# Performance work log

Measured on AMD Instinct MI355X. Metric: run time of the kernel, lower is better.

Reference implementation:

```python
import jax, jax.numpy as jnp
import numpy as np

D_MODEL = 1024
N_HEADS = 16
D_K = D_MODEL // N_HEADS  # 64
B, T = 2, 2048


def setup_inputs() -> dict:
    key = jax.random.key(0)
    ks = jax.random.split(key, 6)
    s = 0.02
    x = jax.random.normal(ks[0], (B, T, D_MODEL), dtype=jnp.float32)
    # Stacked per-head projection weights, [H, C, d_k] (no bias, mini-gpt style)
    Wq = jax.random.normal(ks[1], (N_HEADS, D_MODEL, D_K), dtype=jnp.float32) * s
    Wk = jax.random.normal(ks[2], (N_HEADS, D_MODEL, D_K), dtype=jnp.float32) * s
    Wv = jax.random.normal(ks[3], (N_HEADS, D_MODEL, D_K), dtype=jnp.float32) * s
    # Output projection, torch nn.Linear(d_model, d_model): y = x @ Wo.T + bo
    Wo = jax.random.normal(ks[4], (D_MODEL, D_MODEL), dtype=jnp.float32) * s
    bo = jax.random.normal(ks[5], (D_MODEL,), dtype=jnp.float32) * s
    return {"x": x, "Wq": Wq, "Wk": Wk, "Wv": Wv, "Wo": Wo, "bo": bo}


def reference(x, Wq, Wk, Wv, Wo, bo):
    Bq, Tq, C = x.shape
    # Batched per-head projections (replaces the per-head Python loop)
    q = jnp.einsum('btc,hck->bhtk', x, Wq)  # [B,H,T,dk]
    k = jnp.einsum('btc,hck->bhtk', x, Wk)
    v = jnp.einsum('btc,hck->bhtk', x, Wv)
    scale = 1.0 / jnp.sqrt(jnp.asarray(D_K, dtype=x.dtype))
    scores = jnp.einsum('bhtk,bhsk->bhts', q, k) * scale  # [B,H,T,T]
    causal = jnp.tril(jnp.ones((Tq, Tq), dtype=bool))
    scores = jnp.where(causal, scores, jnp.asarray(-1e9, dtype=scores.dtype))
    attn = jax.nn.softmax(scores, axis=-1)
    out = jnp.einsum('bhts,bhsk->bhtk', attn, v)  # [B,H,T,dk]
    # concat heads -> [B,T,C]
    out = out.transpose(0, 2, 1, 3).reshape(Bq, Tq, C)
    return jnp.einsum('btc,dc->btd', out, Wo) + bo
```

## Files before the change

kernel.cpp:

```cpp
#include <hip/hip_runtime.h>
#include <hip/hip_bf16.h>


using short8 = __attribute__((ext_vector_type(8))) short;
using f32x4  = __attribute__((ext_vector_type(4))) float;
using fp16x2 = __attribute__((ext_vector_type(2))) __fp16;
using half4  = __attribute__((ext_vector_type(4))) _Float16;
using half8  = __attribute__((ext_vector_type(8))) _Float16;

#define SCALE_LOG2E 0.18033688011112042f

__device__ __forceinline__ unsigned short f2bf(float f) {
    union { float f; unsigned u; } v; v.f = f;
    unsigned r = v.u + 0x7fffu + ((v.u >> 16) & 1u);
    return (unsigned short)(r >> 16);
}

__device__ __forceinline__ void gld16(const unsigned short* gp, unsigned short* lp) {
    __builtin_amdgcn_global_load_lds(
        (const __attribute__((address_space(1))) void*)(gp),
        (__attribute__((address_space(3))) void*)(unsigned int)(unsigned long long)(lp),
        16, 0, 0);
}

__global__ void cvt_bf16(const float* __restrict__ in,
                         unsigned short* __restrict__ out, int n4) {
    int i = blockIdx.x * blockDim.x + threadIdx.x;
    if (i >= n4) return;
    float4 v = ((const float4*)in)[i];
    ushort4 o;
    o.x = f2bf(v.x); o.y = f2bf(v.y); o.z = f2bf(v.z); o.w = f2bf(v.w);
    ((ushort4*)out)[i] = o;
}

__global__ void transpose_w(const float* __restrict__ Wq,
                            const float* __restrict__ Wk,
                            const float* __restrict__ Wv,
                            unsigned short* __restrict__ out) {
    __shared__ float tile[64][65];
    int b = blockIdx.x;
    int cchunk = b & 15;
    int h = (b >> 4) & 15;
    int s = b >> 8;
    const float* W = (s == 0) ? Wq : ((s == 1) ? Wk : Wv);
    float sc = (s == 0) ? SCALE_LOG2E : 1.0f;
    const float* src = W + (h * 1024 + cchunk * 64) * 64;
    int t = threadIdx.x;
    #pragma unroll
    for (int it = 0; it < 4; ++it) {
        int idx = (it * 256 + t) * 4;
        int cc = idx >> 6, kk = idx & 63;
        float4 v = *(const float4*)(src + idx);
        tile[cc][kk + 0] = v.x; tile[cc][kk + 1] = v.y;
        tile[cc][kk + 2] = v.z; tile[cc][kk + 3] = v.w;
    }
    __syncthreads();
    unsigned short* dst = out + (size_t)((s * 16 + h) * 64) * 1024 + cchunk * 64;
    #pragma unroll
    for (int it = 0; it < 16; ++it) {
        int idx = it * 256 + t;
        int kk = idx >> 6, cc = idx & 63;
        dst[kk * 1024 + cc] = f2bf(tile[cc][kk] * sc);
    }
}

__global__ __launch_bounds__(256, 5) void qkv_gemm(
        const unsigned short* __restrict__ xb,
        const unsigned short* __restrict__ Wt,
        unsigned short* __restrict__ qB,
        unsigned short* __restrict__ kfrag,
        _Float16* __restrict__ vfrag) {
    __shared__ unsigned short Als[128 * 32];
    __shared__ unsigned short Bls[64 * 32];
    int wave = threadIdx.x >> 6;
    int lane = threadIdx.x & 63;
    int col  = lane & 15;
    int quad = lane >> 4;
    int m_off = (wave & 1) * 64;
    int n_off = (wave >> 1) * 32;
    int ldr = lane >> 2;
    int ldc = ((lane & 3) ^ ((lane >> 3) & 3)) * 8;
    int swq = (quad ^ ((col >> 1) & 3)) * 8;
    int m0 = blockIdx.x * 128;
    int n0 = blockIdx.y * 64;
    f32x4 acc[4][2] = {};
    for (int k0 = 0; k0 < 1024; k0 += 32) {
        __syncthreads();
        #pragma unroll
        for (int j = 0; j < 2; ++j) {
            int row = wave * 32 + j * 16;
            gld16(xb + (size_t)(m0 + row + ldr) * 1024 + k0 + ldc, Als + row * 32);
        }
        {
            int row = wave * 16;
            gld16(Wt + (size_t)(n0 + row + ldr) * 1024 + k0 + ldc, Bls + row * 32);
        }
        __syncthreads();
        short8 af[4], bf[2];
        #pragma unroll
        for (int i = 0; i < 4; ++i)
            af[i] = *(const short8*)(Als + (m_off + i * 16 + col) * 32 + swq);
        #pragma unroll
        for (int i = 0; i < 2; ++i)
            bf[i] = *(const short8*)(Bls + (n_off + i * 16 + col) * 32 + swq);
        #pragma unroll
        for (int mb = 0; mb < 4; ++mb)
            #pragma unroll
            for (int nb = 0; nb < 2; ++nb)
                acc[mb][nb] = __builtin_amdgcn_mfma_f32_16x16x32_bf16(
                    af[mb], bf[nb], acc[mb][nb], 0, 0, 0);
    }
    int sel = blockIdx.y >> 4;
    #pragma unroll
    for (int nb = 0; nb < 2; ++nb) {
        int n = n0 + n_off + nb * 16 + col;
        int d10 = n & 1023;
        int h_ = d10 >> 6, d = d10 & 63;
        if (sel == 0) {
            #pragma unroll
            for (int mb = 0; mb < 4; ++mb)
                #pragma unroll
                for (int r = 0; r < 4; ++r) {
                    int m = m0 + m_off + mb * 16 + quad * 4 + r;
                    int b_ = m >> 11, t_ = m & 2047;
                    qB[((size_t)(b_ * 16 + h_) * 2048 + t_) * 64 + d] =
                        f2bf(acc[mb][nb][r]);
                }
        } else if (sel == 1) {
            int hK = d >> 5, quadk = (d >> 3) & 3, j = d & 7;
            #pragma unroll
            for (int mb = 0; mb < 4; ++mb)
                #pragma unroll
                for (int r = 0; r < 4; ++r) {
                    int m = m0 + m_off + mb * 16 + quad * 4 + r;
                    int b_ = m >> 11, t_ = m & 2047;
                    int bh = b_ * 16 + h_;
                    kfrag[((((size_t)bh * 128 + (t_ >> 4)) * 2 + hK) * 64 +
                           quadk * 16 + (t_ & 15)) * 8 + j] = f2bf(acc[mb][nb][r]);
                }
        } else {
            int nbv = d >> 4, colv = d & 15;
            #pragma unroll
            for (int mb = 0; mb < 4; ++mb) {
                int m = m0 + m_off + mb * 16 + quad * 4;
                int b_ = m >> 11, t_ = m & 2047;
                int bh = b_ * 16 + h_;
                half4 hv;
                hv[0] = (_Float16)acc[mb][nb][0]; hv[1] = (_Float16)acc[mb][nb][1];
                hv[2] = (_Float16)acc[mb][nb][2]; hv[3] = (_Float16)acc[mb][nb][3];
                *(half4*)(vfrag + ((((size_t)bh * 64 + (t_ >> 5)) * 4 + nbv) * 64 +
                          ((t_ >> 2) & 3) * 16 + colv) * 8 + ((t_ >> 4) & 1) * 4) = hv;
            }
        }
    }
}

__global__ __launch_bounds__(256) void oproj(
        const unsigned short* __restrict__ A,
        const unsigned short* __restrict__ Bw,
        const float* __restrict__ bo,
        float* __restrict__ y) {
    __shared__ unsigned short Als[128 * 32];
    __shared__ unsigned short Bls[64 * 32];
    int wave = threadIdx.x >> 6;
    int lane = threadIdx.x & 63;
    int col  = lane & 15;
    int quad = lane >> 4;
    int m_off = (wave & 1) * 64;
    int n_off = (wave >> 1) * 32;
    int ldr = lane >> 2;
    int ldc = ((lane & 3) ^ ((lane >> 3) & 3)) * 8;
    int swq = (quad ^ ((col >> 1) & 3)) * 8;
    int m0 = blockIdx.x * 128;
    int n0 = blockIdx.y * 64;
    f32x4 acc[4][2] = {};
    for (int k0 = 0; k0 < 1024; k0 += 32) {
        __syncthreads();
        #pragma unroll
        for (int j = 0; j < 2; ++j) {
            int row = wave * 32 + j * 16;
            gld16(A + (size_t)(m0 + row + ldr) * 1024 + k0 + ldc, Als + row * 32);
        }
        {
            int row = wave * 16;
            gld16(Bw + (size_t)(n0 + row + ldr) * 1024 + k0 + ldc, Bls + row * 32);
        }
        __syncthreads();
        short8 af[4], bf[2];
        #pragma unroll
        for (int i = 0; i < 4; ++i)
            af[i] = *(const short8*)(Als + (m_off + i * 16 + col) * 32 + swq);
        #pragma unroll
        for (int i = 0; i < 2; ++i)
            bf[i] = *(const short8*)(Bls + (n_off + i * 16 + col) * 32 + swq);
        #pragma unroll
        for (int mb = 0; mb < 4; ++mb)
            #pragma unroll
            for (int nb = 0; nb < 2; ++nb)
                acc[mb][nb] = __builtin_amdgcn_mfma_f32_16x16x32_bf16(
                    af[mb], bf[nb], acc[mb][nb], 0, 0, 0);
    }
    #pragma unroll
    for (int nb = 0; nb < 2; ++nb) {
        int n = n0 + n_off + nb * 16 + col;
        float bias = bo[n];
        #pragma unroll
        for (int mb = 0; mb < 4; ++mb)
            #pragma unroll
            for (int r = 0; r < 4; ++r) {
                int m = m0 + m_off + mb * 16 + quad * 4 + r;
                y[(size_t)m * 1024 + n] = acc[mb][nb][r] + bias;
            }
    }
}

__global__ __launch_bounds__(256, 3) void attn(
        const unsigned short* __restrict__ qB,
        const unsigned short* __restrict__ kfrag,
        const _Float16* __restrict__ vfrag,
        unsigned short* __restrict__ aout) {
    __shared__ float O_comb[2][64][33];
    __shared__ float L_comb[2][2][2][16];
    int wave = threadIdx.x >> 6;
    int lane = threadIdx.x & 63;
    int col  = lane & 15;
    int quad = lane >> 4;
    int sl     = wave >> 1;
    int parity = wave & 1;
    int bh   = blockIdx.x & 31;
    int pairidx = 31 - (blockIdx.x >> 5);
    int strip = pairidx * 2 + sl;
    int q0 = strip * 32;
    const unsigned short* q = qB + (size_t)bh * 2048 * 64;
    const unsigned short* kf_base = kfrag + (size_t)bh * 128 * 2 * 512;
    const _Float16*       vf_base = vfrag + (size_t)bh * 64 * 4 * 512;

    short8 qf[2][2];
    #pragma unroll
    for (int qb = 0; qb < 2; ++qb)
        #pragma unroll
        for (int h = 0; h < 2; ++h)
            qf[qb][h] = *(const short8*)(q + (size_t)(q0 + qb * 16 + col) * 64 + h * 32 + quad * 8);

    f32x4 o[2][4] = {};
    float l[2] = {0.f, 0.f};

    struct KV { short8 kf[2][2]; half8 vv[4]; };
    KV bufA, bufB;

    auto load_half = [&](int it, int kv32, KV& b) {
        int K16 = it * 4 + kv32 * 2;
        #pragma unroll
        for (int p = 0; p < 2; ++p)
            #pragma unroll
            for (int h = 0; h < 2; ++h)
                b.kf[p][h] = *(const short8*)(kf_base +
                    (((size_t)(K16 + p) * 2 + h) * 64 + lane) * 8);
        #pragma unroll
        for (int nb = 0; nb < 4; ++nb)
            b.vv[nb] = *(const half8*)(vf_base +
                (((size_t)(it * 2 + kv32) * 4 + nb) * 64 + lane) * 8);
    };

    auto compute_half = [&](int it, int kv32, KV& b) {
        int kv0 = it * 64;
        bool diag = (kv0 + 63 > q0);
        #pragma unroll
        for (int par = 0; par < 2; ++par) {
            int kvbase = kv0 + kv32 * 32 + par * 16;
            f32x4 st[2] = {};
            #pragma unroll
            for (int qb = 0; qb < 2; ++qb) {
                st[qb] = __builtin_amdgcn_mfma_f32_16x16x32_bf16(b.kf[par][0], qf[qb][0], st[qb], 0, 0, 0);
                st[qb] = __builtin_amdgcn_mfma_f32_16x16x32_bf16(b.kf[par][1], qf[qb][1], st[qb], 0, 0, 0);
            }
            #pragma unroll
            for (int qb = 0; qb < 2; ++qb) {
                float p0 = __builtin_amdgcn_exp2f(st[qb][0]);
                float p1 = __builtin_amdgcn_exp2f(st[qb][1]);
                float p2 = __builtin_amdgcn_exp2f(st[qb][2]);
                float p3 = __builtin_amdgcn_exp2f(st[qb][3]);
                if (diag) {
                    int qg  = q0 + qb * 16 + col;
                    int kvg = kvbase + quad * 4;
                    p0 = (kvg + 0 > qg) ? 0.f : p0;
                    p1 = (kvg + 1 > qg) ? 0.f : p1;
                    p2 = (kvg + 2 > qg) ? 0.f : p2;
                    p3 = (kvg + 3 > qg) ? 0.f : p3;
                }
                l[qb] += (p0 + p1) + (p2 + p3);
                union { fp16x2 h2[2]; half4 h4; } cvt;
                cvt.h2[0] = __builtin_amdgcn_cvt_pkrtz(p0, p1);
                cvt.h2[1] = __builtin_amdgcn_cvt_pkrtz(p2, p3);
                half4 pf = cvt.h4;
                #pragma unroll
                for (int nb = 0; nb < 4; ++nb) {
                    half4 vf = (par == 0)
                        ? __builtin_shufflevector(b.vv[nb], b.vv[nb], 0, 1, 2, 3)
                        : __builtin_shufflevector(b.vv[nb], b.vv[nb], 4, 5, 6, 7);
                    o[qb][nb] = __builtin_amdgcn_mfma_f32_16x16x16f16(pf, vf, o[qb][nb], 0, 0, 0);
                }
            }
        }
    };

    int n_iter = (q0 + 95) >> 6;
    if (parity < n_iter) load_half(parity, 0, bufA);
    for (int it = parity; it < n_iter; it += 2) {
        load_half(it, 1, bufB);
        compute_half(it, 0, bufA);
        if (it + 2 < n_iter) load_half(it + 2, 0, bufA);
        compute_half(it, 1, bufB);
    }

    #pragma unroll
    for (int qb = 0; qb < 2; ++qb) {
        float lr = l[qb];
        lr += __shfl_xor(lr, 16);
        lr += __shfl_xor(lr, 32);
        l[qb] = lr;
    }
    if (quad == 0) {
        L_comb[sl][parity][0][col] = l[0];
        L_comb[sl][parity][1][col] = l[1];
    }
    if (parity == 1) {
        #pragma unroll
        for (int qb = 0; qb < 2; ++qb)
            #pragma unroll
            for (int nb = 0; nb < 4; ++nb)
                #pragma unroll
                for (int r = 0; r < 4; ++r)
                    O_comb[sl][lane][qb * 16 + nb * 4 + r] = o[qb][nb][r];
    }
    __syncthreads();
    if (parity == 0) {
        int b_ = bh >> 4, h_ = bh & 15;
        #pragma unroll
        for (int qb = 0; qb < 2; ++qb)
            #pragma unroll
            for (int r = 0; r < 4; ++r) {
                int qi = quad * 4 + r;
                float inv_l = 1.0f / (L_comb[sl][0][qb][qi] + L_comb[sl][1][qb][qi]);
                int t_ = q0 + qb * 16 + qi;
                #pragma unroll
                for (int nb = 0; nb < 4; ++nb) {
                    float ov = o[qb][nb][r] + O_comb[sl][lane][qb * 16 + nb * 4 + r];
                    aout[(size_t)(b_ * 2048 + t_) * 1024 + h_ * 64 + nb * 16 + col] =
                        f2bf(ov * inv_l);
                }
            }
    }
}

extern "C" void kernel_launch(void* const* d_in, const int* in_sizes, int n_in,
                              void* d_out, int out_size, void* d_ws, size_t ws_size,
                              hipStream_t stream) {
    const float* x  = (const float*)d_in[0];
    const float* Wq = (const float*)d_in[1];
    const float* Wk = (const float*)d_in[2];
    const float* Wv = (const float*)d_in[3];
    const float* Wo = (const float*)d_in[4];
    const float* bo = (const float*)d_in[5];
    float* y = (float*)d_out;

    unsigned short* xb    = (unsigned short*)d_ws;
    unsigned short* Wt    = xb    + 4194304;
    unsigned short* Wob   = Wt    + 3145728;
    unsigned short* qBb   = Wob   + 1048576;
    unsigned short* kfr   = qBb   + 4194304;
    unsigned short* vfr   = kfr   + 4194304;
    unsigned short* aout  = vfr   + 4194304;

    cvt_bf16<<<4096, 256, 0, stream>>>(x,  xb,  1048576);
    cvt_bf16<<<1024, 256, 0, stream>>>(Wo, Wob, 262144);
    transpose_w<<<768, 256, 0, stream>>>(Wq, Wk, Wv, Wt);
    qkv_gemm<<<dim3(32, 48), 256, 0, stream>>>(xb, Wt, qBb, kfr, (_Float16*)vfr);
    attn<<<1024, 256, 0, stream>>>(qBb, kfr, (const _Float16*)vfr, aout);
    oproj<<<dim3(32, 16), 256, 0, stream>>>(aout, Wob, bo, y);
}
```

Before: 179.1 us.

## Pre-swizzle weights into MFMA fragment layout and load B directly to registers

The weight preprocessing kernels now write Wq/Wk/Wv and Wo in an MFMA-fragment-major bf16 layout, so the GEMMs load B operands straight from global memory into registers with one coalesced 16-byte load per lane and skip the LDS staging. The QKV and output-projection GEMMs are retiled to 128-thread blocks where each wave owns a 64-wide N slice. The aim is less LDS traffic and fewer barriers per K step, and more blocks for the output projection. The cost is that B fragments are no longer shared across waves through LDS, and the direct global loads sit in the loop without prefetching.

```diff
diff --git a/kernel.cpp b/kernel.cpp
--- a/kernel.cpp
+++ b/kernel.cpp
@@ -36,7 +36,7 @@
 __global__ void transpose_w(const float* __restrict__ Wq,
                             const float* __restrict__ Wk,
                             const float* __restrict__ Wv,
-                            unsigned short* __restrict__ out) {
+                            unsigned short* __restrict__ wfrag) {
     __shared__ float tile[64][65];
     int b = blockIdx.x;
     int cchunk = b & 15;
@@ -55,65 +55,91 @@
         tile[cc][kk + 2] = v.z; tile[cc][kk + 3] = v.w;
     }
     __syncthreads();
-    unsigned short* dst = out + (size_t)((s * 16 + h) * 64) * 1024 + cchunk * 64;
-    #pragma unroll
-    for (int it = 0; it < 16; ++it) {
-        int idx = it * 256 + t;
-        int kk = idx >> 6, cc = idx & 63;
-        dst[kk * 1024 + cc] = f2bf(tile[cc][kk] * sc);
-    }
-}
-
-__global__ __launch_bounds__(256, 5) void qkv_gemm(
+    int sh = s * 16 + h;
+    #pragma unroll
+    for (int p = 0; p < 2; ++p) {
+        int slot = p * 256 + t;
+        int d   = slot & 63;
+        int cc8 = slot >> 6;
+        int n16  = sh * 4 + (d >> 4);
+        int col  = d & 15;
+        int kq   = cchunk * 2 + (cc8 >> 2);
+        int quad = cc8 & 3;
+        ushort4 lo, hi;
+        lo.x = f2bf(tile[cc8 * 8 + 0][d] * sc); lo.y = f2bf(tile[cc8 * 8 + 1][d] * sc);
+        lo.z = f2bf(tile[cc8 * 8 + 2][d] * sc); lo.w = f2bf(tile[cc8 * 8 + 3][d] * sc);
+        hi.x = f2bf(tile[cc8 * 8 + 4][d] * sc); hi.y = f2bf(tile[cc8 * 8 + 5][d] * sc);
+        hi.z = f2bf(tile[cc8 * 8 + 6][d] * sc); hi.w = f2bf(tile[cc8 * 8 + 7][d] * sc);
+        unsigned short* dst = wfrag + ((size_t)((n16 * 32 + kq) * 64 + quad * 16 + col)) * 8;
+        *(ushort4*)dst = lo;
+        *(ushort4*)(dst + 4) = hi;
+    }
+}
+
+__global__ void wo_frag(const float* __restrict__ Wo,
+                        unsigned short* __restrict__ wofrag) {
+    int g = blockIdx.x * 256 + threadIdx.x;
+    int col  = g & 15;
+    int quad = (g >> 4) & 3;
+    int kq   = (g >> 6) & 31;
+    int n16  = g >> 11;
+    const float* src = Wo + (size_t)(n16 * 16 + col) * 1024 + kq * 32 + quad * 8;
+    float4 a = *(const float4*)src;
+    float4 b = *(const float4*)(src + 4);
+    ushort4 lo, hi;
+    lo.x = f2bf(a.x); lo.y = f2bf(a.y); lo.z = f2bf(a.z); lo.w = f2bf(a.w);
+    hi.x = f2bf(b.x); hi.y = f2bf(b.y); hi.z = f2bf(b.z); hi.w = f2bf(b.w);
+    *(ushort4*)(wofrag + (size_t)g * 8)     = lo;
+    *(ushort4*)(wofrag + (size_t)g * 8 + 4) = hi;
+}
+
+__global__ __launch_bounds__(128, 4) void qkv_gemm(
         const unsigned short* __restrict__ xb,
-        const unsigned short* __restrict__ Wt,
+        const unsigned short* __restrict__ wtf,
         unsigned short* __restrict__ qB,
         unsigned short* __restrict__ kfrag,
         _Float16* __restrict__ vfrag) {
-    __shared__ unsigned short Als[128 * 32];
-    __shared__ unsigned short Bls[64 * 32];
+    __shared__ unsigned short Als[64 * 32];
     int wave = threadIdx.x >> 6;
     int lane = threadIdx.x & 63;
     int col  = lane & 15;
     int quad = lane >> 4;
-    int m_off = (wave & 1) * 64;
-    int n_off = (wave >> 1) * 32;
     int ldr = lane >> 2;
     int ldc = ((lane & 3) ^ ((lane >> 3) & 3)) * 8;
     int swq = (quad ^ ((col >> 1) & 3)) * 8;
-    int m0 = blockIdx.x * 128;
-    int n0 = blockIdx.y * 64;
-    f32x4 acc[4][2] = {};
+    int m0 = blockIdx.x * 64;
+    int n0 = blockIdx.y * 128 + wave * 64;
+    int n16b = n0 >> 4;
+    f32x4 acc[4][4] = {};
     for (int k0 = 0; k0 < 1024; k0 += 32) {
+        int kq = k0 >> 5;
         __syncthreads();
+        short8 bf[4];
+        #pragma unroll
+        for (int nb = 0; nb < 4; ++nb)
+            bf[nb] = *(const short8*)(wtf +
+                ((size_t)((n16b + nb) * 32 + kq) * 64 + lane) * 8);
         #pragma unroll
         for (int j = 0; j < 2; ++j) {
             int row = wave * 32 + j * 16;
             gld16(xb + (size_t)(m0 + row + ldr) * 1024 + k0 + ldc, Als + row * 32);
         }
-        {
-            int row = wave * 16;
-            gld16(Wt + (size_t)(n0 + row + ldr) * 1024 + k0 + ldc, Bls + row * 32);
-        }
         __syncthreads();
-        short8 af[4], bf[2];
+        short8 af[4];
         #pragma unroll
         for (int i = 0; i < 4; ++i)
-            af[i] = *(const short8*)(Als + (m_off + i * 16 + col) * 32 + swq);
-        #pragma unroll
-        for (int i = 0; i < 2; ++i)
-            bf[i] = *(const short8*)(Bls + (n_off + i * 16 + col) * 32 + swq);
+            af[i] = *(const short8*)(Als + (i * 16 + col) * 32 + swq);
         #pragma unroll
         for (int mb = 0; mb < 4; ++mb)
             #pragma unroll
-            for (int nb = 0; nb < 2; ++nb)
+            for (int nb = 0; nb < 4; ++nb)
                 acc[mb][nb] = __builtin_amdgcn_mfma_f32_16x16x32_bf16(
                     af[mb], bf[nb], acc[mb][nb], 0, 0, 0);
     }
-    int sel = blockIdx.y >> 4;
-    #pragma unroll
-    for (int nb = 0; nb < 2; ++nb) {
-        int n = n0 + n_off + nb * 16 + col;
+    int sel = blockIdx.y >> 3;
+    #pragma unroll
+    for (int nb = 0; nb < 4; ++nb) {
+        int n = n0 + nb * 16 + col;
         int d10 = n & 1023;
         int h_ = d10 >> 6, d = d10 & 63;
         if (sel == 0) {
@@ -121,7 +147,7 @@
             for (int mb = 0; mb < 4; ++mb)
                 #pragma unroll
                 for (int r = 0; r < 4; ++r) {
-                    int m = m0 + m_off + mb * 16 + quad * 4 + r;
+                    int m = m0 + mb * 16 + quad * 4 + r;
                     int b_ = m >> 11, t_ = m & 2047;
                     qB[((size_t)(b_ * 16 + h_) * 2048 + t_) * 64 + d] =
                         f2bf(acc[mb][nb][r]);
@@ -132,7 +158,7 @@
             for (int mb = 0; mb < 4; ++mb)
                 #pragma unroll
                 for (int r = 0; r < 4; ++r) {
-                    int m = m0 + m_off + mb * 16 + quad * 4 + r;
+                    int m = m0 + mb * 16 + quad * 4 + r;
                     int b_ = m >> 11, t_ = m & 2047;
                     int bh = b_ * 16 + h_;
                     kfrag[((((size_t)bh * 128 + (t_ >> 4)) * 2 + hK) * 64 +
@@ -142,7 +168,7 @@
             int nbv = d >> 4, colv = d & 15;
             #pragma unroll
             for (int mb = 0; mb < 4; ++mb) {
-                int m = m0 + m_off + mb * 16 + quad * 4;
+                int m = m0 + mb * 16 + quad * 4;
                 int b_ = m >> 11, t_ = m & 2047;
                 int bh = b_ * 16 + h_;
                 half4 hv;
@@ -155,60 +181,54 @@
     }
 }
 
-__global__ __launch_bounds__(256) void oproj(
+__global__ __launch_bounds__(128, 4) void oproj(
         const unsigned short* __restrict__ A,
-        const unsigned short* __restrict__ Bw,
+        const unsigned short* __restrict__ wof,
         const float* __restrict__ bo,
         float* __restrict__ y) {
-    __shared__ unsigned short Als[128 * 32];
-    __shared__ unsigned short Bls[64 * 32];
+    __shared__ unsigned short Als[32 * 32];
     int wave = threadIdx.x >> 6;
     int lane = threadIdx.x & 63;
     int col  = lane & 15;
     int quad = lane >> 4;
-    int m_off = (wave & 1) * 64;
-    int n_off = (wave >> 1) * 32;
     int ldr = lane >> 2;
     int ldc = ((lane & 3) ^ ((lane >> 3) & 3)) * 8;
     int swq = (quad ^ ((col >> 1) & 3)) * 8;
-    int m0 = blockIdx.x * 128;
-    int n0 = blockIdx.y * 64;
-    f32x4 acc[4][2] = {};
+    int m0 = blockIdx.x * 32;
+    int n0 = blockIdx.y * 128 + wave * 64;
+    int n16b = n0 >> 4;
+    f32x4 acc[2][4] = {};
     for (int k0 = 0; k0 < 1024; k0 += 32) {
+        int kq = k0 >> 5;
         __syncthreads();
-        #pragma unroll
-        for (int j = 0; j < 2; ++j) {
-            int row = wave * 32 + j * 16;
-            gld16(A + (size_t)(m0 + row + ldr) * 1024 + k0 + ldc, Als + row * 32);
-        }
-        {
-            int row = wave * 16;
-            gld16(Bw + (size_t)(n0 + row + ldr) * 1024 + k0 + ldc, Bls + row * 32);
-        }
+        short8 bf[4];
+        #pragma unroll
+        for (int nb = 0; nb < 4; ++nb)
+            bf[nb] = *(const short8*)(wof +
+                ((size_t)((n16b + nb) * 32 + kq) * 64 + lane) * 8);
+        gld16(A + (size_t)(m0 + wave * 16 + ldr) * 1024 + k0 + ldc,
+              Als + (wave * 16) * 32);
         __syncthreads();
-        short8 af[4], bf[2];
-        #pragma unroll
-        for (int i = 0; i < 4; ++i)
-            af[i] = *(const short8*)(Als + (m_off + i * 16 + col) * 32 + swq);
+        short8 af[2];
         #pragma unroll
         for (int i = 0; i < 2; ++i)
-            bf[i] = *(const short8*)(Bls + (n_off + i * 16 + col) * 32 + swq);
-        #pragma unroll
-        for (int mb = 0; mb < 4; ++mb)
-            #pragma unroll
-            for (int nb = 0; nb < 2; ++nb)
+            af[i] = *(const short8*)(Als + (i * 16 + col) * 32 + swq);
+        #pragma unroll
+        for (int mb = 0; mb < 2; ++mb)
+            #pragma unroll
+            for (int nb = 0; nb < 4; ++nb)
                 acc[mb][nb] = __builtin_amdgcn_mfma_f32_16x16x32_bf16(
                     af[mb], bf[nb], acc[mb][nb], 0, 0, 0);
     }
     #pragma unroll
-    for (int nb = 0; nb < 2; ++nb) {
-        int n = n0 + n_off + nb * 16 + col;
+    for (int nb = 0; nb < 4; ++nb) {
+        int n = n0 + nb * 16 + col;
         float bias = bo[n];
         #pragma unroll
-        for (int mb = 0; mb < 4; ++mb)
+        for (int mb = 0; mb < 2; ++mb)
             #pragma unroll
             for (int r = 0; r < 4; ++r) {
-                int m = m0 + m_off + mb * 16 + quad * 4 + r;
+                int m = m0 + mb * 16 + quad * 4 + r;
                 y[(size_t)m * 1024 + n] = acc[mb][nb][r] + bias;
             }
     }
@@ -365,17 +385,17 @@
     float* y = (float*)d_out;
 
     unsigned short* xb    = (unsigned short*)d_ws;
-    unsigned short* Wt    = xb    + 4194304;
-    unsigned short* Wob   = Wt    + 3145728;
-    unsigned short* qBb   = Wob   + 1048576;
+    unsigned short* Wtf   = xb    + 4194304;
+    unsigned short* Wof   = Wtf   + 3145728;
+    unsigned short* qBb   = Wof   + 1048576;
     unsigned short* kfr   = qBb   + 4194304;
     unsigned short* vfr   = kfr   + 4194304;
     unsigned short* aout  = vfr   + 4194304;
 
-    cvt_bf16<<<4096, 256, 0, stream>>>(x,  xb,  1048576);
-    cvt_bf16<<<1024, 256, 0, stream>>>(Wo, Wob, 262144);
-    transpose_w<<<768, 256, 0, stream>>>(Wq, Wk, Wv, Wt);
-    qkv_gemm<<<dim3(32, 48), 256, 0, stream>>>(xb, Wt, qBb, kfr, (_Float16*)vfr);
+    cvt_bf16<<<4096, 256, 0, stream>>>(x, xb, 1048576);
+    transpose_w<<<768, 256, 0, stream>>>(Wq, Wk, Wv, Wtf);
+    wo_frag<<<512, 256, 0, stream>>>(Wo, Wof);
+    qkv_gemm<<<dim3(64, 24), 128, 0, stream>>>(xb, Wtf, qBb, kfr, (_Float16*)vfr);
     attn<<<1024, 256, 0, stream>>>(qBb, kfr, (const _Float16*)vfr, aout);
-    oproj<<<dim3(32, 16), 256, 0, stream>>>(aout, Wob, bo, y);
-}
+    oproj<<<dim3(128, 8), 128, 0, stream>>>(aout, Wof, bo, y);
+}
```

Result: faster. 170.4 us (-4.9%).
